# Kernel tuning notes

Measured on AMD Instinct MI355X. Metric: run time of the kernel, lower is better.

## Reference

```python
import jax, jax.numpy as jnp
import numpy as np

B, R, L, K, E, H, V, QV = 256, 6, 10, 49, 300, 512, 2001, 10000


def _lstm_dir(x, Wih, Whh, bih, bhh):
    # x: [N, L, E]; returns final hidden state [N, H] (PyTorch gate order i,f,g,o)
    N = x.shape[0]
    Hd = Whh.shape[1]
    b = bih + bhh

    def step(carry, xt):
        h, c = carry
        gates = xt @ Wih.T + h @ Whh.T + b
        i, f, g, o = jnp.split(gates, 4, axis=-1)
        c = jax.nn.sigmoid(f) * c + jax.nn.sigmoid(i) * jnp.tanh(g)
        h = jax.nn.sigmoid(o) * jnp.tanh(c)
        return (h, c), None

    init = (jnp.zeros((N, Hd), x.dtype), jnp.zeros((N, Hd), x.dtype))
    (h, _), _ = jax.lax.scan(step, init, jnp.swapaxes(x, 0, 1))
    return h


def setup_inputs() -> dict:
    key = jax.random.key(0)
    ks = jax.random.split(key, 40)
    s = 0.02
    d = {}
    d['img'] = jax.random.normal(ks[0], (B * R, K, H), jnp.float32)
    d['role_qs'] = jax.random.randint(ks[1], (B, R, L), 0, QV, jnp.int64)
    d['qword_emb'] = jax.random.normal(ks[2], (QV, E), jnp.float32) * s
    d['lstm_Wih_f'] = jax.random.normal(ks[3], (4 * H, E), jnp.float32) * s
    d['lstm_Whh_f'] = jax.random.normal(ks[4], (4 * H, H), jnp.float32) * s
    d['lstm_bih_f'] = jnp.zeros((4 * H,), jnp.float32)
    d['lstm_bhh_f'] = jnp.zeros((4 * H,), jnp.float32)
    d['lstm_Wih_b'] = jax.random.normal(ks[5], (4 * H, E), jnp.float32) * s
    d['lstm_Whh_b'] = jax.random.normal(ks[6], (4 * H, H), jnp.float32) * s
    d['lstm_bih_b'] = jnp.zeros((4 * H,), jnp.float32)
    d['lstm_bhh_b'] = jnp.zeros((4 * H,), jnp.float32)
    d['proj_W'] = jax.random.normal(ks[7], (H, 2 * H), jnp.float32) * s
    d['proj_b'] = jnp.zeros((H,), jnp.float32)
    d['vatt_vW'] = jax.random.normal(ks[8], (H, H), jnp.float32) * s
    d['vatt_vb'] = jnp.zeros((H,), jnp.float32)
    d['vatt_qW'] = jax.random.normal(ks[9], (H, H), jnp.float32) * s
    d['vatt_qb'] = jnp.zeros((H,), jnp.float32)
    d['vatt_oW'] = jax.random.normal(ks[10], (1, H), jnp.float32) * s
    d['vatt_ob'] = jnp.zeros((1,), jnp.float32)
    d['qnet_W'] = jax.random.normal(ks[11], (H, H), jnp.float32) * s
    d['qnet_b'] = jnp.zeros((H,), jnp.float32)
    d['vnet_W'] = jax.random.normal(ks[12], (H, H), jnp.float32) * s
    d['vnet_b'] = jnp.zeros((H,), jnp.float32)
    d['cls_W1'] = jax.random.normal(ks[13], (2 * H, H), jnp.float32) * s
    d['cls_b1'] = jnp.zeros((2 * H,), jnp.float32)
    d['cls_W2'] = jax.random.normal(ks[14], (V, 2 * H), jnp.float32) * s
    d['cls_b2'] = jnp.zeros((V,), jnp.float32)
    d['g0_W'] = jax.random.normal(ks[15], (H, 2 * H), jnp.float32) * s
    d['g0_b'] = jnp.zeros((H,), jnp.float32)
    d['g1_W'] = jax.random.normal(ks[16], (H, H), jnp.float32) * s
    d['g1_b'] = jnp.zeros((H,), jnp.float32)
    d['g2_W'] = jax.random.normal(ks[17], (H, H), jnp.float32) * s
    d['g2_b'] = jnp.zeros((H,), jnp.float32)
    d['g3_W'] = jax.random.normal(ks[18], (H, H), jnp.float32) * s
    d['g3_b'] = jnp.zeros((H,), jnp.float32)
    d['f0_W'] = jax.random.normal(ks[19], (H, H), jnp.float32) * s
    d['f0_b'] = jnp.zeros((H,), jnp.float32)
    d['f1_W'] = jax.random.normal(ks[20], (H, H), jnp.float32) * s
    d['f1_b'] = jnp.zeros((H,), jnp.float32)
    return d


def _forward(img, qword_emb,
             lstm_Wih_f, lstm_Whh_f, lstm_bih_f, lstm_bhh_f,
             lstm_Wih_b, lstm_Whh_b, lstm_bih_b, lstm_bhh_b,
             proj_W, proj_b, vatt_vW, vatt_vb, vatt_qW, vatt_qb, vatt_oW, vatt_ob,
             qnet_W, qnet_b, vnet_W, vnet_b, cls_W1, cls_b1, cls_W2, cls_b2,
             g0_W, g0_b, g1_W, g1_b, g2_W, g2_b, g3_W, g3_b,
             f0_W, f0_b, f1_W, f1_b, role_qs):
    relu = jax.nn.relu
    bsz, roles = role_qs.shape[0], role_qs.shape[1]
    toks = role_qs.reshape(-1, role_qs.shape[-1])          # [B*R, L]
    w_emb = qword_emb[toks]                                 # [B*R, L, E]
    # bidirectional LSTM final hidden states
    h_f = _lstm_dir(w_emb, lstm_Wih_f, lstm_Whh_f, lstm_bih_f, lstm_bhh_f)
    h_b = _lstm_dir(w_emb[:, ::-1, :], lstm_Wih_b, lstm_Whh_b, lstm_bih_b, lstm_bhh_b)
    q_emb = jnp.concatenate([h_f, h_b], axis=-1) @ proj_W.T + proj_b   # [B*R, H]
    # top-down attention over image regions
    v_proj = relu(img @ vatt_vW.T + vatt_vb)                # [B*R, K, H]
    q_proj = relu(q_emb @ vatt_qW.T + vatt_qb)              # [B*R, H]
    att_logits = (v_proj * q_proj[:, None, :]) @ vatt_oW.T + vatt_ob  # [B*R, K, 1]
    att = jax.nn.softmax(att_logits, axis=1)
    v_emb = jnp.sum(att * img, axis=1)                      # [B*R, H]
    # joint representation + answer classifier
    q_repr = relu(q_emb @ qnet_W.T + qnet_b)
    v_repr = relu(v_emb @ vnet_W.T + vnet_b)
    joint_repr = q_repr * v_repr                            # [B*R, H]
    logits = relu(joint_repr @ cls_W1.T + cls_b1) @ cls_W2.T + cls_b2  # [B*R, V]
    # relation network over pairwise role representations
    jr = joint_repr.reshape(bsz, roles, -1)                 # [B, R, H]
    r1 = jnp.broadcast_to(jr[:, None, :, :], (bsz, roles, roles, jr.shape[-1]))
    r2 = jnp.broadcast_to(jr[:, :, None, :], (bsz, roles, roles, jr.shape[-1]))
    cat = jnp.concatenate([r1, r2], axis=-1).reshape(-1, 2 * jr.shape[-1])  # [B*R*R, 2H]
    g = relu(cat @ g0_W.T + g0_b)
    g = relu(g @ g1_W.T + g1_b)
    g = relu(g @ g2_W.T + g2_b)
    g = relu(g @ g3_W.T + g3_b)
    g = g.reshape(bsz, roles * roles, -1).sum(axis=1)       # [B, H]
    rec = relu(g @ f0_W.T + f0_b) @ f1_W.T + f1_b           # [B, H]
    rec = rec / jnp.sqrt(jnp.sum(rec * rec, axis=1, keepdims=True))  # l2norm
    return logits, rec


def reference(img, role_qs, qword_emb,
              lstm_Wih_f, lstm_Whh_f, lstm_bih_f, lstm_bhh_f,
              lstm_Wih_b, lstm_Whh_b, lstm_bih_b, lstm_bhh_b,
              proj_W, proj_b, vatt_vW, vatt_vb, vatt_qW, vatt_qb, vatt_oW, vatt_ob,
              qnet_W, qnet_b, vnet_W, vnet_b, cls_W1, cls_b1, cls_W2, cls_b2,
              g0_W, g0_b, g1_W, g1_b, g2_W, g2_b, g3_W, g3_b,
              f0_W, f0_b, f1_W, f1_b):
    return _forward(img, qword_emb,
                    lstm_Wih_f, lstm_Whh_f, lstm_bih_f, lstm_bhh_f,
                    lstm_Wih_b, lstm_Whh_b, lstm_bih_b, lstm_bhh_b,
                    proj_W, proj_b, vatt_vW, vatt_vb, vatt_qW, vatt_qb, vatt_oW, vatt_ob,
                    qnet_W, qnet_b, vnet_W, vnet_b, cls_W1, cls_b1, cls_W2, cls_b2,
                    g0_W, g0_b, g1_W, g1_b, g2_W, g2_b, g3_W, g3_b,
                    f0_W, f0_b, f1_W, f1_b, role_qs)
```

## Files before the change

### kernel.cpp

```cpp
#include <hip/hip_runtime.h>
#include <hip/hip_bf16.h>
#include <math.h>

typedef __attribute__((ext_vector_type(8))) short short8;
typedef __attribute__((ext_vector_type(4))) float f32x4;

#define BT 64
#define KTILE 32
#define LSTR 40

__device__ __forceinline__ short8 cvt8(const float* x) {
    short8 r;
#pragma unroll
    for (int i = 0; i < 8; ++i) {
        __hip_bfloat16 b = __float2bfloat16(x[i]);
        r[i] = *reinterpret_cast<const short*>(&b);
    }
    return r;
}

__global__ __launch_bounds__(256)
void mfma_gemm_kernel(const float* __restrict__ A1, const int* __restrict__ idx1, int idx_stride,
                      int lda1, int k1,
                      const float* __restrict__ W1, int ldw1,
                      const float* __restrict__ A2, int lda2, int k2,
                      const float* __restrict__ W2, int ldw2,
                      const float* __restrict__ bias1, const float* __restrict__ bias2,
                      const float* __restrict__ mulvec, const float* __restrict__ mul,
                      float* __restrict__ C, int ldc, int M, int N, int do_relu, int mode)
{
    __shared__ short sA[2][BT][LSTR];
    __shared__ short sB[2][BT][LSTR];
    __shared__ float sred[BT][2];

    const int tid = threadIdx.x;
    int m0, n0, ch8 = 0;
    if (mode == 1) {
        const int xcd = blockIdx.x & 7;
        const int gi = xcd * 1176 + (blockIdx.x >> 3);
        m0 = (gi >> 3) << 6;
        ch8 = gi & 7;
        n0 = ch8 << 6;
    } else {
        m0 = blockIdx.y * BT;
        n0 = blockIdx.x * BT;
    }
    const int Ktot = k1 + k2;
    const int srow = tid >> 2;
    const int skq  = (tid & 3) << 3;
    const int lane = tid & 63;
    const int wave = tid >> 6;
    const int wr = (wave >> 1) << 5;
    const int wc = (wave & 1) << 5;
    const int l15 = lane & 15;
    const int lh  = lane >> 4;

    const int rg = min(m0 + srow, M - 1);
    const int arow = idx1 ? idx1[(size_t)rg * idx_stride] : rg;
    const int ng = min(n0 + srow, N - 1);

    f32x4 acc[2][2];
#pragma unroll
    for (int m = 0; m < 2; ++m)
#pragma unroll
        for (int n = 0; n < 2; ++n)
            acc[m][n] = (f32x4){0.f, 0.f, 0.f, 0.f};

    const int nt = (Ktot + KTILE - 1) / KTILE;
    float a[8], w[8];

    auto loadregs = [&](int t) {
        const int kb = t * KTILE;
        if (kb + KTILE <= k1) {
            const float* p = A1 + (size_t)arow * lda1 + kb + skq;
            float4 v0 = *(const float4*)p, v1 = *(const float4*)(p + 4);
            a[0]=v0.x; a[1]=v0.y; a[2]=v0.z; a[3]=v0.w; a[4]=v1.x; a[5]=v1.y; a[6]=v1.z; a[7]=v1.w;
            const float* q = W1 + (size_t)ng * ldw1 + kb + skq;
            float4 u0 = *(const float4*)q, u1 = *(const float4*)(q + 4);
            w[0]=u0.x; w[1]=u0.y; w[2]=u0.z; w[3]=u0.w; w[4]=u1.x; w[5]=u1.y; w[6]=u1.z; w[7]=u1.w;
        } else if (kb >= k1 && kb + KTILE <= Ktot) {
            const float* p = A2 + (size_t)rg * lda2 + (kb - k1) + skq;
            float4 v0 = *(const float4*)p, v1 = *(const float4*)(p + 4);
            a[0]=v0.x; a[1]=v0.y; a[2]=v0.z; a[3]=v0.w; a[4]=v1.x; a[5]=v1.y; a[6]=v1.z; a[7]=v1.w;
            const float* q = W2 + (size_t)ng * ldw2 + (kb - k1) + skq;
            float4 u0 = *(const float4*)q, u1 = *(const float4*)(q + 4);
            w[0]=u0.x; w[1]=u0.y; w[2]=u0.z; w[3]=u0.w; w[4]=u1.x; w[5]=u1.y; w[6]=u1.z; w[7]=u1.w;
        } else {
#pragma unroll
            for (int e = 0; e < 8; ++e) {
                int kg = kb + skq + e;
                float av = 0.f, wv = 0.f;
                if (kg < k1) {
                    av = A1[(size_t)arow * lda1 + kg];
                    wv = W1[(size_t)ng * ldw1 + kg];
                } else if (kg < Ktot) {
                    av = A2[(size_t)rg * lda2 + (kg - k1)];
                    wv = W2[(size_t)ng * ldw2 + (kg - k1)];
                }
                a[e] = av; w[e] = wv;
            }
        }
    };
    auto cvtwrite = [&](int buf) {
        *(short8*)&sA[buf][srow][skq] = cvt8(a);
        *(short8*)&sB[buf][srow][skq] = cvt8(w);
    };

    loadregs(0);
    cvtwrite(0);
    __syncthreads();

    for (int t = 0; t < nt; ++t) {
        const int cur = t & 1;
        if (t + 1 < nt) loadregs(t + 1);
        short8 af[2], bf[2];
#pragma unroll
        for (int m = 0; m < 2; ++m)
            af[m] = *(const short8*)&sA[cur][wr + (m << 4) + l15][lh << 3];
#pragma unroll
        for (int n = 0; n < 2; ++n)
            bf[n] = *(const short8*)&sB[cur][wc + (n << 4) + l15][lh << 3];
#pragma unroll
        for (int m = 0; m < 2; ++m)
#pragma unroll
            for (int n = 0; n < 2; ++n)
                acc[m][n] = __builtin_amdgcn_mfma_f32_16x16x32_bf16(af[m], bf[n], acc[m][n], 0, 0, 0);
        if (t + 1 < nt) cvtwrite(cur ^ 1);
        __syncthreads();
    }

    if (mode == 0) {
#pragma unroll
        for (int m = 0; m < 2; ++m) {
#pragma unroll
            for (int j = 0; j < 4; ++j) {
                const int r = m0 + wr + (m << 4) + (lh << 2) + j;
                if (r >= M) continue;
#pragma unroll
                for (int n = 0; n < 2; ++n) {
                    const int c = n0 + wc + (n << 4) + l15;
                    if (c >= N) continue;
                    float v = acc[m][n][j];
                    if (bias1) v += bias1[c];
                    if (bias2) v += bias2[c];
                    if (do_relu) v = fmaxf(v, 0.f);
                    if (mulvec) v *= mulvec[c];
                    if (mul) v *= mul[(size_t)r * ldc + c];
                    C[(size_t)r * ldc + c] = v;
                }
            }
        }
    } else {
#pragma unroll
        for (int m = 0; m < 2; ++m) {
#pragma unroll
            for (int j = 0; j < 4; ++j) {
                const int rloc = wr + (m << 4) + (lh << 2) + j;
                const int r = m0 + rloc;
                const size_t sqbase = (size_t)(r / 49) * ldc;
                float s = 0.f;
#pragma unroll
                for (int n = 0; n < 2; ++n) {
                    const int c = n0 + wc + (n << 4) + l15;
                    float v = acc[m][n][j] + bias1[c];
                    v = fmaxf(v, 0.f);
                    s += v * mul[sqbase + c];
                }
                s += __shfl_xor(s, 1, 64);
                s += __shfl_xor(s, 2, 64);
                s += __shfl_xor(s, 4, 64);
                s += __shfl_xor(s, 8, 64);
                if (l15 == 0) sred[rloc][wc >> 5] = s;
            }
        }
        __syncthreads();
        if (tid < BT)
            C[(size_t)(m0 + tid) * 8 + ch8] = sred[tid][0] + sred[tid][1];
    }
}

__global__ __launch_bounds__(256)
void lstm_reorder_kernel(const float* __restrict__ Wih, const float* __restrict__ Whh,
                         const float* __restrict__ bih, const float* __restrict__ bhh,
                         short* __restrict__ Wbf, float* __restrict__ bias_perm)
{
    int id = blockIdx.x * 256 + threadIdx.x;
    int c = id >> 9, k = id & 511;
    int src = (c & 3) * 512 + (c >> 2);
    {
        __hip_bfloat16 b = __float2bfloat16(Whh[(size_t)src * 512 + k]);
        Wbf[(size_t)c * 832 + k] = *(short*)&b;
    }
    if (k < 300) {
        __hip_bfloat16 b = __float2bfloat16(Wih[(size_t)src * 300 + k]);
        Wbf[(size_t)c * 832 + 512 + k] = *(short*)&b;
    } else if (k < 320) {
        Wbf[(size_t)c * 832 + 512 + k] = 0;
    }
    if (k == 0) bias_perm[c] = bih[src] + bhh[src];
}

__global__ __launch_bounds__(256)
void lstm_step2_kernel(const float* __restrict__ hF_in, const float* __restrict__ hB_in,
                       const short* __restrict__ WbfF, const short* __restrict__ WbfB,
                       const float* __restrict__ biasF, const float* __restrict__ biasB,
                       const float* __restrict__ emb, const int* __restrict__ toks,
                       int tF, int tB,
                       float* __restrict__ hF_out, float* __restrict__ hB_out,
                       float* __restrict__ cF, float* __restrict__ cB)
{
    __shared__ short sA[2][BT][LSTR];
    __shared__ short sB[2][BT][LSTR];
    const int dir = blockIdx.z;
    const float* h_in = dir ? hB_in : hF_in;
    const short* Wbf  = dir ? WbfB : WbfF;
    const float* bias_perm = dir ? biasB : biasF;
    float* h_out  = dir ? hB_out : hF_out;
    float* cstate = dir ? cB : cF;
    const int tt = dir ? tB : tF;

    const int tid = threadIdx.x;
    const int m0 = blockIdx.y << 6;
    const int n0 = blockIdx.x << 6;
    const int srow = tid >> 2, skq = (tid & 3) << 3;
    const int lane = tid & 63, wave = tid >> 6;
    const int wr = (wave >> 1) << 5, wc = (wave & 1) << 5;
    const int l15 = lane & 15, lh = lane >> 4;
    const int Ktot = 812;
    const int nt = 26;
    const int rg = m0 + srow;
    const int ng = n0 + srow;
    const int arow = toks[rg * 10 + tt];

    f32x4 acc[2][2];
#pragma unroll
    for (int m = 0; m < 2; ++m)
#pragma unroll
        for (int n = 0; n < 2; ++n)
            acc[m][n] = (f32x4){0.f, 0.f, 0.f, 0.f};

    float a[8];
    short8 wb;
    auto loadregs = [&](int t) {
        const int kb = t << 5;
        wb = *(const short8*)&Wbf[(size_t)ng * 832 + kb + skq];
        const int k0 = kb + skq;
        if (k0 + 8 <= 512) {
            const float* p = h_in + ((size_t)rg << 9) + k0;
            float4 v0 = *(const float4*)p, v1 = *(const float4*)(p + 4);
            a[0]=v0.x; a[1]=v0.y; a[2]=v0.z; a[3]=v0.w; a[4]=v1.x; a[5]=v1.y; a[6]=v1.z; a[7]=v1.w;
        } else if (k0 + 8 <= Ktot) {
            const float* p = emb + (size_t)arow * 300 + (k0 - 512);
            float4 v0 = *(const float4*)p, v1 = *(const float4*)(p + 4);
            a[0]=v0.x; a[1]=v0.y; a[2]=v0.z; a[3]=v0.w; a[4]=v1.x; a[5]=v1.y; a[6]=v1.z; a[7]=v1.w;
        } else {
#pragma unroll
            for (int e = 0; e < 8; ++e) {
                int kg = k0 + e;
                a[e] = (kg < 512) ? h_in[((size_t)rg << 9) + kg]
                                  : (kg < Ktot ? emb[(size_t)arow * 300 + (kg - 512)] : 0.f);
            }
        }
    };
    auto cvtwrite = [&](int buf) {
        *(short8*)&sA[buf][srow][skq] = cvt8(a);
        *(short8*)&sB[buf][srow][skq] = wb;
    };

    loadregs(0);
    cvtwrite(0);
    __syncthreads();
    for (int t = 0; t < nt; ++t) {
        const int cur = t & 1;
        if (t + 1 < nt) loadregs(t + 1);
        short8 af[2], bf[2];
#pragma unroll
        for (int m = 0; m < 2; ++m)
            af[m] = *(const short8*)&sA[cur][wr + (m << 4) + l15][lh << 3];
#pragma unroll
        for (int n = 0; n < 2; ++n)
            bf[n] = *(const short8*)&sB[cur][wc + (n << 4) + l15][lh << 3];
#pragma unroll
        for (int m = 0; m < 2; ++m)
#pragma unroll
            for (int n = 0; n < 2; ++n)
                acc[m][n] = __builtin_amdgcn_mfma_f32_16x16x32_bf16(af[m], bf[n], acc[m][n], 0, 0, 0);
        if (t + 1 < nt) cvtwrite(cur ^ 1);
        __syncthreads();
    }

#pragma unroll
    for (int n = 0; n < 2; ++n) {
        const int ccol = n0 + wc + (n << 4) + l15;
        const float bb = bias_perm[ccol];
        const int u = ccol >> 2;
#pragma unroll
        for (int m = 0; m < 2; ++m) {
#pragma unroll
            for (int j = 0; j < 4; ++j) {
                const int r = m0 + wr + (m << 4) + (lh << 2) + j;
                float v = acc[m][n][j] + bb;
                const int base = lane & ~3;
                float gi = __shfl(v, base, 64);
                float gf = __shfl(v, base | 1, 64);
                float gg = __shfl(v, base | 2, 64);
                float go = __shfl(v, base | 3, 64);
                if ((lane & 3) == 0) {
                    float si = 1.f / (1.f + expf(-gi));
                    float sf = 1.f / (1.f + expf(-gf));
                    float so = 1.f / (1.f + expf(-go));
                    size_t idx = ((size_t)r << 9) + u;
                    float cv = sf * cstate[idx] + si * tanhf(gg);
                    cstate[idx] = cv;
                    h_out[idx] = so * tanhf(cv);
                }
            }
        }
    }
}

__global__ __launch_bounds__(256)
void attn_vemb_kernel(const float* __restrict__ partial, const float* __restrict__ img,
                      float* __restrict__ v_emb)
{
    __shared__ float satt[49];
    const int n = blockIdx.x;
    const int tid = threadIdx.x;
    if (tid < 64) {
        float v = -1e30f;
        if (tid < 49) {
            const float* pp = partial + ((size_t)n * 49 + tid) * 8;
            v = ((pp[0] + pp[1]) + (pp[2] + pp[3])) + ((pp[4] + pp[5]) + (pp[6] + pp[7]));
        }
        float m = v;
#pragma unroll
        for (int off = 32; off; off >>= 1) m = fmaxf(m, __shfl_xor(m, off, 64));
        float e = (tid < 49) ? expf(v - m) : 0.f;
        float s = e;
#pragma unroll
        for (int off = 32; off; off >>= 1) s += __shfl_xor(s, off, 64);
        if (tid < 49) satt[tid] = e / s;
    }
    __syncthreads();
    const float2* ip = (const float2*)(img + (size_t)n * 49 * 512);
    float2 s2 = make_float2(0.f, 0.f);
    for (int k = 0; k < 49; ++k) {
        float2 v = ip[k * 256 + tid];
        float a = satt[k];
        s2.x = fmaf(a, v.x, s2.x);
        s2.y = fmaf(a, v.y, s2.y);
    }
    ((float2*)(v_emb + (size_t)n * 512))[tid] = s2;
}

__global__ __launch_bounds__(256)
void g0build_kernel(const float* __restrict__ P, const float* __restrict__ Q,
                    const float* __restrict__ b0, float* __restrict__ g0)
{
    int id = blockIdx.x * 256 + threadIdx.x;
    int cc = id & 511;
    int r = id >> 9;
    int j = r % 6;
    int t = r / 6;
    int i = t % 6;
    int b = t / 6;
    float v = P[((size_t)(b * 6 + j) << 9) + cc] + Q[((size_t)(b * 6 + i) << 9) + cc] + b0[cc];
    g0[id] = fmaxf(v, 0.f);
}

__global__ __launch_bounds__(256)
void gsum_kernel(const float* __restrict__ g, float* __restrict__ out)
{
    int id = blockIdx.x * 256 + threadIdx.x;
    int b = id >> 9, hh = id & 511;
    const float* p = g + (size_t)b * 36 * 512 + hh;
    float s = 0.f;
#pragma unroll
    for (int i = 0; i < 36; ++i) s += p[i * 512];
    out[id] = s;
}

__global__ __launch_bounds__(256)
void l2norm_kernel(const float* __restrict__ in, float* __restrict__ out)
{
    int b = blockIdx.x;
    int tid = threadIdx.x;
    float v0 = in[(size_t)b * 512 + tid];
    float v1 = in[(size_t)b * 512 + 256 + tid];
    float s = v0 * v0 + v1 * v1;
#pragma unroll
    for (int off = 32; off; off >>= 1) s += __shfl_down(s, off, 64);
    __shared__ float ps[4];
    if ((tid & 63) == 0) ps[tid >> 6] = s;
    __syncthreads();
    float tot = ps[0] + ps[1] + ps[2] + ps[3];
    float inv = 1.f / sqrtf(tot);
    out[(size_t)b * 512 + tid] = v0 * inv;
    out[(size_t)b * 512 + 256 + tid] = v1 * inv;
}

extern "C" void kernel_launch(void* const* d_in, const int* in_sizes, int n_in,
                              void* d_out, int out_size, void* d_ws, size_t ws_size,
                              hipStream_t stream)
{
    (void)in_sizes; (void)n_in; (void)out_size; (void)ws_size;
    const float* img    = (const float*)d_in[0];
    const int*   toks   = (const int*)d_in[1];
    const float* qword  = (const float*)d_in[2];
    const float* Wih_f  = (const float*)d_in[3];
    const float* Whh_f  = (const float*)d_in[4];
    const float* bih_f  = (const float*)d_in[5];
    const float* bhh_f  = (const float*)d_in[6];
    const float* Wih_b  = (const float*)d_in[7];
    const float* Whh_b  = (const float*)d_in[8];
    const float* bih_b  = (const float*)d_in[9];
    const float* bhh_b  = (const float*)d_in[10];
    const float* proj_W = (const float*)d_in[11];
    const float* proj_b = (const float*)d_in[12];
    const float* vatt_vW = (const float*)d_in[13];
    const float* vatt_vb = (const float*)d_in[14];
    const float* vatt_qW = (const float*)d_in[15];
    const float* vatt_qb = (const float*)d_in[16];
    const float* vatt_oW = (const float*)d_in[17];
    const float* qnet_W = (const float*)d_in[19];
    const float* qnet_b = (const float*)d_in[20];
    const float* vnet_W = (const float*)d_in[21];
    const float* vnet_b = (const float*)d_in[22];
    const float* cls_W1 = (const float*)d_in[23];
    const float* cls_b1 = (const float*)d_in[24];
    const float* cls_W2 = (const float*)d_in[25];
    const float* cls_b2 = (const float*)d_in[26];
    const float* g0_W   = (const float*)d_in[27];
    const float* g0_b   = (const float*)d_in[28];
    const float* g1_W   = (const float*)d_in[29];
    const float* g1_b   = (const float*)d_in[30];
    const float* g2_W   = (const float*)d_in[31];
    const float* g2_b   = (const float*)d_in[32];
    const float* g3_W   = (const float*)d_in[33];
    const float* g3_b   = (const float*)d_in[34];
    const float* f0_W   = (const float*)d_in[35];
    const float* f0_b   = (const float*)d_in[36];
    const float* f1_W   = (const float*)d_in[37];
    const float* f1_b   = (const float*)d_in[38];

    float* out_logits = (float*)d_out;
    float* out_rec    = (float*)d_out + 1536 * 2001;

    const size_t FB = 786432;
    float* zone = (float*)d_ws;
    float* gA    = zone;
    float* gB    = zone + 4718592;
    float* hid1  = zone + 9437184;
    float* Pb    = zone + 11010048;
    float* Qb    = zone + 11796480;
    float* gsumb = zone + 12582912;
    float* f0o   = zone + 12713984;
    float* rectb = zone + 12845056;
    float* p = zone + 12976128;
    auto alloc = [&](size_t nf) { float* q = p; p += nf; return q; };
    float* hP0   = alloc(FB);
    float* hP2   = alloc(FB);
    float* joint = alloc(FB);
    float* partial = alloc(602112);
    short* WbfF  = (short*)alloc(851968);
    short* WbfB  = (short*)alloc(851968);
    float* biasF = alloc(2048);
    float* biasB = alloc(2048);
    float* hP1 = gA;
    float* hP3 = gA + FB;
    float* cF  = gA + 2 * FB;
    float* cB  = gA + 3 * FB;
    float* q_emb  = Pb;
    float* swq    = hid1;
    float* q_repr = gA;
    float* v_emb  = gA + FB;

    auto gemm = [&](const float* A1, const int* idx1, int idxs, int lda1, int k1,
                    const float* W1, int ldw1,
                    const float* A2, int lda2, int k2, const float* W2, int ldw2,
                    const float* b1, const float* b2, const float* mv, const float* mulp,
                    float* Cp, int ldc, int M, int N, int relu) {
        dim3 g((N + BT - 1) / BT, (M + BT - 1) / BT);
        hipLaunchKernelGGL(mfma_gemm_kernel, g, dim3(256), 0, stream,
                           A1, idx1, idxs, lda1, k1, W1, ldw1, A2, lda2, k2, W2, ldw2,
                           b1, b2, mv, mulp, Cp, ldc, M, N, relu, 0);
    };

    const int NR = 1536;
    hipLaunchKernelGGL(lstm_reorder_kernel, dim3(4096), dim3(256), 0, stream,
                       Wih_f, Whh_f, bih_f, bhh_f, WbfF, biasF);
    hipLaunchKernelGGL(lstm_reorder_kernel, dim3(4096), dim3(256), 0, stream,
                       Wih_b, Whh_b, bih_b, bhh_b, WbfB, biasB);
    hipMemsetAsync(hP0, 0, FB * sizeof(float), stream);
    hipMemsetAsync(hP2, 0, FB * sizeof(float), stream);
    hipMemsetAsync(cF, 0, FB * sizeof(float), stream);
    hipMemsetAsync(cB, 0, FB * sizeof(float), stream);
    {
        float *fi = hP0, *fo = hP1, *bi = hP2, *bo = hP3;
        for (int t = 0; t < 10; ++t) {
            hipLaunchKernelGGL(lstm_step2_kernel, dim3(32, 24, 2), dim3(256), 0, stream,
                               fi, bi, WbfF, WbfB, biasF, biasB, qword, toks, t, 9 - t,
                               fo, bo, cF, cB);
            float* tmp = fi; fi = fo; fo = tmp;
            tmp = bi; bi = bo; bo = tmp;
        }
    }

    gemm(hP0, nullptr, 0, 512, 512, proj_W, 1024,
         hP2, 512, 512, proj_W + 512, 1024,
         proj_b, nullptr, nullptr, nullptr, q_emb, 512, NR, 512, 0);
    gemm(q_emb, nullptr, 0, 512, 512, vatt_qW, 512, nullptr, 0, 0, nullptr, 0,
         vatt_qb, nullptr, vatt_oW, nullptr, swq, 512, NR, 512, 1);
    hipLaunchKernelGGL(mfma_gemm_kernel, dim3(9408), dim3(256), 0, stream,
                       img, (const int*)nullptr, 0, 512, 512, vatt_vW, 512,
                       (const float*)nullptr, 0, 0, (const float*)nullptr, 0,
                       vatt_vb, (const float*)nullptr, (const float*)nullptr, swq,
                       partial, 512, 75264, 512, 0, 1);
    hipLaunchKernelGGL(attn_vemb_kernel, dim3(1536), dim3(256), 0, stream,
                       partial, img, v_emb);
    gemm(q_emb, nullptr, 0, 512, 512, qnet_W, 512, nullptr, 0, 0, nullptr, 0,
         qnet_b, nullptr, nullptr, nullptr, q_repr, 512, NR, 512, 1);
    gemm(v_emb, nullptr, 0, 512, 512, vnet_W, 512, nullptr, 0, 0, nullptr, 0,
         vnet_b, nullptr, nullptr, q_repr, joint, 512, NR, 512, 1);
    gemm(joint, nullptr, 0, 512, 512, cls_W1, 512, nullptr, 0, 0, nullptr, 0,
         cls_b1, nullptr, nullptr, nullptr, hid1, 1024, NR, 1024, 1);
    gemm(hid1, nullptr, 0, 1024, 1024, cls_W2, 1024, nullptr, 0, 0, nullptr, 0,
         cls_b2, nullptr, nullptr, nullptr, out_logits, 2001, NR, 2001, 0);
    gemm(joint, nullptr, 0, 512, 512, g0_W, 1024, nullptr, 0, 0, nullptr, 0,
         nullptr, nullptr, nullptr, nullptr, Pb, 512, NR, 512, 0);
    gemm(joint, nullptr, 0, 512, 512, g0_W + 512, 1024, nullptr, 0, 0, nullptr, 0,
         nullptr, nullptr, nullptr, nullptr, Qb, 512, NR, 512, 0);
    hipLaunchKernelGGL(g0build_kernel, dim3(18432), dim3(256), 0, stream, Pb, Qb, g0_b, gA);
    gemm(gA, nullptr, 0, 512, 512, g1_W, 512, nullptr, 0, 0, nullptr, 0,
         g1_b, nullptr, nullptr, nullptr, gB, 512, 9216, 512, 1);
    gemm(gB, nullptr, 0, 512, 512, g2_W, 512, nullptr, 0, 0, nullptr, 0,
         g2_b, nullptr, nullptr, nullptr, gA, 512, 9216, 512, 1);
    gemm(gA, nullptr, 0, 512, 512, g3_W, 512, nullptr, 0, 0, nullptr, 0,
         g3_b, nullptr, nullptr, nullptr, gB, 512, 9216, 512, 1);
    hipLaunchKernelGGL(gsum_kernel, dim3(512), dim3(256), 0, stream, gB, gsumb);
    gemm(gsumb, nullptr, 0, 512, 512, f0_W, 512, nullptr, 0, 0, nullptr, 0,
         f0_b, nullptr, nullptr, nullptr, f0o, 512, 256, 512, 1);
    gemm(f0o, nullptr, 0, 512, 512, f1_W, 512, nullptr, 0, 0, nullptr, 0,
         f1_b, nullptr, nullptr, nullptr, rectb, 512, 256, 512, 0);
    hipLaunchKernelGGL(l2norm_kernel, dim3(256), dim3(256), 0, stream, rectb, out_rec);
}
```

Measured before the change: 941.6 us.

## Store intermediate activations in bf16 and enlarge GEMM tiles to 128x64

Intermediate activations (LSTM hidden states, g-MLP buffers, joint and hidden layers) are now written and read as bf16 rather than fp32. The image tensor is pre-converted to bf16 when workspace permits. The GEMM and LSTM step kernels move from 64x64 to 128x64 tiles, with each wave computing 4x2 MFMA tiles. The goal is to halve activation memory traffic and conversion work and to raise per-block compute reuse, at the cost of an extra image conversion pass, more registers, and fewer blocks.

```diff
diff --git a/kernel.cpp b/kernel.cpp
--- a/kernel.cpp
+++ b/kernel.cpp
@@ -5,7 +5,6 @@
 typedef __attribute__((ext_vector_type(8))) short short8;
 typedef __attribute__((ext_vector_type(4))) float f32x4;
 
-#define BT 64
 #define KTILE 32
 #define LSTR 40
 
@@ -18,120 +17,152 @@
     }
     return r;
 }
-
-__global__ __launch_bounds__(256)
-void mfma_gemm_kernel(const float* __restrict__ A1, const int* __restrict__ idx1, int idx_stride,
-                      int lda1, int k1,
+__device__ __forceinline__ float bf2f(short s) {
+    unsigned int u = ((unsigned int)(unsigned short)s) << 16;
+    return __uint_as_float(u);
+}
+
+__global__ __launch_bounds__(256)
+void mfma_gemm_kernel(const float* __restrict__ A1f, int lda1, int k1,
                       const float* __restrict__ W1, int ldw1,
-                      const float* __restrict__ A2, int lda2, int k2,
+                      const float* __restrict__ A2f, int lda2, int k2,
                       const float* __restrict__ W2, int ldw2,
                       const float* __restrict__ bias1, const float* __restrict__ bias2,
                       const float* __restrict__ mulvec, const float* __restrict__ mul,
-                      float* __restrict__ C, int ldc, int M, int N, int do_relu, int mode)
-{
-    __shared__ short sA[2][BT][LSTR];
-    __shared__ short sB[2][BT][LSTR];
-    __shared__ float sred[BT][2];
+                      float* __restrict__ C, int ldc, int M, int N,
+                      int do_relu, int mode, int abits, int c_bf16)
+{
+    __shared__ short sA[2][128][LSTR];
+    __shared__ short sB[2][64][LSTR];
+    __shared__ float sred[128][2];
 
     const int tid = threadIdx.x;
     int m0, n0, ch8 = 0;
     if (mode == 1) {
         const int xcd = blockIdx.x & 7;
-        const int gi = xcd * 1176 + (blockIdx.x >> 3);
-        m0 = (gi >> 3) << 6;
+        const int gi = xcd * 588 + (blockIdx.x >> 3);
+        m0 = (gi >> 3) << 7;
         ch8 = gi & 7;
         n0 = ch8 << 6;
     } else {
-        m0 = blockIdx.y * BT;
-        n0 = blockIdx.x * BT;
-    }
+        m0 = blockIdx.y << 7;
+        n0 = blockIdx.x << 6;
+    }
+    const short* A1b = (const short*)A1f;
+    const short* A2b = (const short*)A2f;
     const int Ktot = k1 + k2;
-    const int srow = tid >> 2;
-    const int skq  = (tid & 3) << 3;
-    const int lane = tid & 63;
-    const int wave = tid >> 6;
-    const int wr = (wave >> 1) << 5;
+    const int nt = (Ktot + KTILE - 1) / KTILE;
+    const int lane = tid & 63, wave = tid >> 6;
+    const int wr = (wave >> 1) << 6;
     const int wc = (wave & 1) << 5;
-    const int l15 = lane & 15;
-    const int lh  = lane >> 4;
-
-    const int rg = min(m0 + srow, M - 1);
-    const int arow = idx1 ? idx1[(size_t)rg * idx_stride] : rg;
-    const int ng = min(n0 + srow, N - 1);
-
-    f32x4 acc[2][2];
-#pragma unroll
-    for (int m = 0; m < 2; ++m)
-#pragma unroll
-        for (int n = 0; n < 2; ++n)
-            acc[m][n] = (f32x4){0.f, 0.f, 0.f, 0.f};
-
-    const int nt = (Ktot + KTILE - 1) / KTILE;
-    float a[8], w[8];
-
-    auto loadregs = [&](int t) {
-        const int kb = t * KTILE;
-        if (kb + KTILE <= k1) {
-            const float* p = A1 + (size_t)arow * lda1 + kb + skq;
-            float4 v0 = *(const float4*)p, v1 = *(const float4*)(p + 4);
-            a[0]=v0.x; a[1]=v0.y; a[2]=v0.z; a[3]=v0.w; a[4]=v1.x; a[5]=v1.y; a[6]=v1.z; a[7]=v1.w;
-            const float* q = W1 + (size_t)ng * ldw1 + kb + skq;
+    const int l15 = lane & 15, lh = lane >> 4;
+    const int rowA = tid >> 1, kA = (tid & 1) << 4;
+    const int rgA = min(m0 + rowA, M - 1);
+    const int rowW = tid >> 2, kW = (tid & 3) << 3;
+    const int ngW = min(n0 + rowW, N - 1);
+
+    f32x4 acc[4][2];
+#pragma unroll
+    for (int m = 0; m < 4; ++m)
+#pragma unroll
+        for (int n = 0; n < 2; ++n) acc[m][n] = (f32x4){0.f, 0.f, 0.f, 0.f};
+
+    short8 aS0, aS1, wS;
+    auto loadA = [&](int t) {
+        const int k0 = t * KTILE + kA;
+        if (k0 + 16 <= k1) {
+            if (abits & 1) {
+                const short* p = A1b + (size_t)rgA * lda1 + k0;
+                aS0 = *(const short8*)p; aS1 = *(const short8*)(p + 8);
+            } else {
+                const float* p = A1f + (size_t)rgA * lda1 + k0;
+                float4 v0 = *(const float4*)p, v1 = *(const float4*)(p + 4);
+                float4 v2 = *(const float4*)(p + 8), v3 = *(const float4*)(p + 12);
+                float t0[8] = {v0.x, v0.y, v0.z, v0.w, v1.x, v1.y, v1.z, v1.w};
+                float t1[8] = {v2.x, v2.y, v2.z, v2.w, v3.x, v3.y, v3.z, v3.w};
+                aS0 = cvt8(t0); aS1 = cvt8(t1);
+            }
+        } else if (k0 >= k1 && k0 + 16 <= Ktot) {
+            const int kk = k0 - k1;
+            if (abits & 2) {
+                const short* p = A2b + (size_t)rgA * lda2 + kk;
+                aS0 = *(const short8*)p; aS1 = *(const short8*)(p + 8);
+            } else {
+                const float* p = A2f + (size_t)rgA * lda2 + kk;
+                float4 v0 = *(const float4*)p, v1 = *(const float4*)(p + 4);
+                float4 v2 = *(const float4*)(p + 8), v3 = *(const float4*)(p + 12);
+                float t0[8] = {v0.x, v0.y, v0.z, v0.w, v1.x, v1.y, v1.z, v1.w};
+                float t1[8] = {v2.x, v2.y, v2.z, v2.w, v3.x, v3.y, v3.z, v3.w};
+                aS0 = cvt8(t0); aS1 = cvt8(t1);
+            }
+        } else {
+            float tmp[16];
+#pragma unroll
+            for (int e = 0; e < 16; ++e) {
+                const int kg = k0 + e;
+                float v = 0.f;
+                if (kg < k1) v = (abits & 1) ? bf2f(A1b[(size_t)rgA * lda1 + kg]) : A1f[(size_t)rgA * lda1 + kg];
+                else if (kg < Ktot) v = (abits & 2) ? bf2f(A2b[(size_t)rgA * lda2 + (kg - k1)]) : A2f[(size_t)rgA * lda2 + (kg - k1)];
+                tmp[e] = v;
+            }
+            aS0 = cvt8(tmp); aS1 = cvt8(tmp + 8);
+        }
+    };
+    auto loadW = [&](int t) {
+        const int k0 = t * KTILE + kW;
+        if (k0 + 8 <= k1) {
+            const float* q = W1 + (size_t)ngW * ldw1 + k0;
             float4 u0 = *(const float4*)q, u1 = *(const float4*)(q + 4);
-            w[0]=u0.x; w[1]=u0.y; w[2]=u0.z; w[3]=u0.w; w[4]=u1.x; w[5]=u1.y; w[6]=u1.z; w[7]=u1.w;
-        } else if (kb >= k1 && kb + KTILE <= Ktot) {
-            const float* p = A2 + (size_t)rg * lda2 + (kb - k1) + skq;
-            float4 v0 = *(const float4*)p, v1 = *(const float4*)(p + 4);
-            a[0]=v0.x; a[1]=v0.y; a[2]=v0.z; a[3]=v0.w; a[4]=v1.x; a[5]=v1.y; a[6]=v1.z; a[7]=v1.w;
-            const float* q = W2 + (size_t)ng * ldw2 + (kb - k1) + skq;
+            float t0[8] = {u0.x, u0.y, u0.z, u0.w, u1.x, u1.y, u1.z, u1.w};
+            wS = cvt8(t0);
+        } else if (k0 >= k1 && k0 + 8 <= Ktot) {
+            const float* q = W2 + (size_t)ngW * ldw2 + (k0 - k1);
             float4 u0 = *(const float4*)q, u1 = *(const float4*)(q + 4);
-            w[0]=u0.x; w[1]=u0.y; w[2]=u0.z; w[3]=u0.w; w[4]=u1.x; w[5]=u1.y; w[6]=u1.z; w[7]=u1.w;
+            float t0[8] = {u0.x, u0.y, u0.z, u0.w, u1.x, u1.y, u1.z, u1.w};
+            wS = cvt8(t0);
         } else {
+            float tmp[8];
 #pragma unroll
             for (int e = 0; e < 8; ++e) {
-                int kg = kb + skq + e;
-                float av = 0.f, wv = 0.f;
-                if (kg < k1) {
-                    av = A1[(size_t)arow * lda1 + kg];
-                    wv = W1[(size_t)ng * ldw1 + kg];
-                } else if (kg < Ktot) {
-                    av = A2[(size_t)rg * lda2 + (kg - k1)];
-                    wv = W2[(size_t)ng * ldw2 + (kg - k1)];
-                }
-                a[e] = av; w[e] = wv;
-            }
+                const int kg = k0 + e;
+                float v = 0.f;
+                if (kg < k1) v = W1[(size_t)ngW * ldw1 + kg];
+                else if (kg < Ktot) v = W2[(size_t)ngW * ldw2 + (kg - k1)];
+                tmp[e] = v;
+            }
+            wS = cvt8(tmp);
         }
     };
-    auto cvtwrite = [&](int buf) {
-        *(short8*)&sA[buf][srow][skq] = cvt8(a);
-        *(short8*)&sB[buf][srow][skq] = cvt8(w);
+    auto writeS = [&](int buf) {
+        *(short8*)&sA[buf][rowA][kA] = aS0;
+        *(short8*)&sA[buf][rowA][kA + 8] = aS1;
+        *(short8*)&sB[buf][rowW][kW] = wS;
     };
 
-    loadregs(0);
-    cvtwrite(0);
+    loadA(0); loadW(0); writeS(0);
     __syncthreads();
-
     for (int t = 0; t < nt; ++t) {
         const int cur = t & 1;
-        if (t + 1 < nt) loadregs(t + 1);
-        short8 af[2], bf[2];
-#pragma unroll
-        for (int m = 0; m < 2; ++m)
+        if (t + 1 < nt) { loadA(t + 1); loadW(t + 1); }
+        short8 af[4], bfv[2];
+#pragma unroll
+        for (int m = 0; m < 4; ++m)
             af[m] = *(const short8*)&sA[cur][wr + (m << 4) + l15][lh << 3];
 #pragma unroll
         for (int n = 0; n < 2; ++n)
-            bf[n] = *(const short8*)&sB[cur][wc + (n << 4) + l15][lh << 3];
-#pragma unroll
-        for (int m = 0; m < 2; ++m)
+            bfv[n] = *(const short8*)&sB[cur][wc + (n << 4) + l15][lh << 3];
+#pragma unroll
+        for (int m = 0; m < 4; ++m)
 #pragma unroll
             for (int n = 0; n < 2; ++n)
-                acc[m][n] = __builtin_amdgcn_mfma_f32_16x16x32_bf16(af[m], bf[n], acc[m][n], 0, 0, 0);
-        if (t + 1 < nt) cvtwrite(cur ^ 1);
+                acc[m][n] = __builtin_amdgcn_mfma_f32_16x16x32_bf16(af[m], bfv[n], acc[m][n], 0, 0, 0);
+        if (t + 1 < nt) writeS(cur ^ 1);
         __syncthreads();
     }
 
     if (mode == 0) {
 #pragma unroll
-        for (int m = 0; m < 2; ++m) {
+        for (int m = 0; m < 4; ++m) {
 #pragma unroll
             for (int j = 0; j < 4; ++j) {
                 const int r = m0 + wr + (m << 4) + (lh << 2) + j;
@@ -146,13 +177,18 @@
                     if (do_relu) v = fmaxf(v, 0.f);
                     if (mulvec) v *= mulvec[c];
                     if (mul) v *= mul[(size_t)r * ldc + c];
-                    C[(size_t)r * ldc + c] = v;
+                    if (c_bf16) {
+                        __hip_bfloat16 b = __float2bfloat16(v);
+                        ((short*)C)[(size_t)r * ldc + c] = *(short*)&b;
+                    } else {
+                        C[(size_t)r * ldc + c] = v;
+                    }
                 }
             }
         }
     } else {
 #pragma unroll
-        for (int m = 0; m < 2; ++m) {
+        for (int m = 0; m < 4; ++m) {
 #pragma unroll
             for (int j = 0; j < 4; ++j) {
                 const int rloc = wr + (m << 4) + (lh << 2) + j;
@@ -174,7 +210,7 @@
             }
         }
         __syncthreads();
-        if (tid < BT)
+        if (tid < 128)
             C[(size_t)(m0 + tid) * 8 + ch8] = sred[tid][0] + sred[tid][1];
     }
 }
@@ -201,91 +237,94 @@
 }
 
 __global__ __launch_bounds__(256)
-void lstm_step2_kernel(const float* __restrict__ hF_in, const float* __restrict__ hB_in,
+void lstm_step2_kernel(const short* __restrict__ hF_in, const short* __restrict__ hB_in,
                        const short* __restrict__ WbfF, const short* __restrict__ WbfB,
                        const float* __restrict__ biasF, const float* __restrict__ biasB,
                        const float* __restrict__ emb, const int* __restrict__ toks,
                        int tF, int tB,
-                       float* __restrict__ hF_out, float* __restrict__ hB_out,
+                       short* __restrict__ hF_out, short* __restrict__ hB_out,
                        float* __restrict__ cF, float* __restrict__ cB)
 {
-    __shared__ short sA[2][BT][LSTR];
-    __shared__ short sB[2][BT][LSTR];
+    __shared__ short sA[2][128][LSTR];
+    __shared__ short sB[2][64][LSTR];
     const int dir = blockIdx.z;
-    const float* h_in = dir ? hB_in : hF_in;
+    const short* h_in = dir ? hB_in : hF_in;
     const short* Wbf  = dir ? WbfB : WbfF;
     const float* bias_perm = dir ? biasB : biasF;
-    float* h_out  = dir ? hB_out : hF_out;
+    short* h_out  = dir ? hB_out : hF_out;
     float* cstate = dir ? cB : cF;
     const int tt = dir ? tB : tF;
 
     const int tid = threadIdx.x;
-    const int m0 = blockIdx.y << 6;
+    const int m0 = blockIdx.y << 7;
     const int n0 = blockIdx.x << 6;
-    const int srow = tid >> 2, skq = (tid & 3) << 3;
     const int lane = tid & 63, wave = tid >> 6;
-    const int wr = (wave >> 1) << 5, wc = (wave & 1) << 5;
+    const int wr = (wave >> 1) << 6, wc = (wave & 1) << 5;
     const int l15 = lane & 15, lh = lane >> 4;
-    const int Ktot = 812;
+    const int rowA = tid >> 1, kA = (tid & 1) << 4;
+    const int rgA = m0 + rowA;
+    const int rowW = tid >> 2, kW = (tid & 3) << 3;
+    const int ngW = n0 + rowW;
     const int nt = 26;
-    const int rg = m0 + srow;
-    const int ng = n0 + srow;
-    const int arow = toks[rg * 10 + tt];
-
-    f32x4 acc[2][2];
-#pragma unroll
-    for (int m = 0; m < 2; ++m)
-#pragma unroll
-        for (int n = 0; n < 2; ++n)
-            acc[m][n] = (f32x4){0.f, 0.f, 0.f, 0.f};
-
-    float a[8];
-    short8 wb;
-    auto loadregs = [&](int t) {
-        const int kb = t << 5;
-        wb = *(const short8*)&Wbf[(size_t)ng * 832 + kb + skq];
-        const int k0 = kb + skq;
-        if (k0 + 8 <= 512) {
-            const float* p = h_in + ((size_t)rg << 9) + k0;
-            float4 v0 = *(const float4*)p, v1 = *(const float4*)(p + 4);
-            a[0]=v0.x; a[1]=v0.y; a[2]=v0.z; a[3]=v0.w; a[4]=v1.x; a[5]=v1.y; a[6]=v1.z; a[7]=v1.w;
-        } else if (k0 + 8 <= Ktot) {
+    const int arow = toks[rgA * 10 + tt];
+
+    f32x4 acc[4][2];
+#pragma unroll
+    for (int m = 0; m < 4; ++m)
+#pragma unroll
+        for (int n = 0; n < 2; ++n) acc[m][n] = (f32x4){0.f, 0.f, 0.f, 0.f};
+
+    short8 aS0, aS1, wS;
+    auto loadA = [&](int t) {
+        const int k0 = (t << 5) + kA;
+        if (k0 + 16 <= 512) {
+            const short* p = h_in + (size_t)rgA * 512 + k0;
+            aS0 = *(const short8*)p; aS1 = *(const short8*)(p + 8);
+        } else if (k0 >= 512 && k0 + 16 <= 812) {
             const float* p = emb + (size_t)arow * 300 + (k0 - 512);
             float4 v0 = *(const float4*)p, v1 = *(const float4*)(p + 4);
-            a[0]=v0.x; a[1]=v0.y; a[2]=v0.z; a[3]=v0.w; a[4]=v1.x; a[5]=v1.y; a[6]=v1.z; a[7]=v1.w;
+            float4 v2 = *(const float4*)(p + 8), v3 = *(const float4*)(p + 12);
+            float t0[8] = {v0.x, v0.y, v0.z, v0.w, v1.x, v1.y, v1.z, v1.w};
+            float t1[8] = {v2.x, v2.y, v2.z, v2.w, v3.x, v3.y, v3.z, v3.w};
+            aS0 = cvt8(t0); aS1 = cvt8(t1);
         } else {
-#pragma unroll
-            for (int e = 0; e < 8; ++e) {
-                int kg = k0 + e;
-                a[e] = (kg < 512) ? h_in[((size_t)rg << 9) + kg]
-                                  : (kg < Ktot ? emb[(size_t)arow * 300 + (kg - 512)] : 0.f);
-            }
+            float tmp[16];
+#pragma unroll
+            for (int e = 0; e < 16; ++e) {
+                const int kg = k0 + e;
+                tmp[e] = (kg < 812) ? ((kg < 512) ? bf2f(h_in[(size_t)rgA * 512 + kg])
+                                                  : emb[(size_t)arow * 300 + (kg - 512)]) : 0.f;
+            }
+            aS0 = cvt8(tmp); aS1 = cvt8(tmp + 8);
         }
     };
-    auto cvtwrite = [&](int buf) {
-        *(short8*)&sA[buf][srow][skq] = cvt8(a);
-        *(short8*)&sB[buf][srow][skq] = wb;
+    auto loadW = [&](int t) {
+        wS = *(const short8*)&Wbf[(size_t)ngW * 832 + (t << 5) + kW];
     };
-
-    loadregs(0);
-    cvtwrite(0);
+    auto writeS = [&](int buf) {
+        *(short8*)&sA[buf][rowA][kA] = aS0;
+        *(short8*)&sA[buf][rowA][kA + 8] = aS1;
+        *(short8*)&sB[buf][rowW][kW] = wS;
+    };
+
+    loadA(0); loadW(0); writeS(0);
     __syncthreads();
     for (int t = 0; t < nt; ++t) {
         const int cur = t & 1;
-        if (t + 1 < nt) loadregs(t + 1);
-        short8 af[2], bf[2];
-#pragma unroll
-        for (int m = 0; m < 2; ++m)
+        if (t + 1 < nt) { loadA(t + 1); loadW(t + 1); }
+        short8 af[4], bfv[2];
+#pragma unroll
+        for (int m = 0; m < 4; ++m)
             af[m] = *(const short8*)&sA[cur][wr + (m << 4) + l15][lh << 3];
 #pragma unroll
         for (int n = 0; n < 2; ++n)
-            bf[n] = *(const short8*)&sB[cur][wc + (n << 4) + l15][lh << 3];
-#pragma unroll
-        for (int m = 0; m < 2; ++m)
+            bfv[n] = *(const short8*)&sB[cur][wc + (n << 4) + l15][lh << 3];
+#pragma unroll
+        for (int m = 0; m < 4; ++m)
 #pragma unroll
             for (int n = 0; n < 2; ++n)
-                acc[m][n] = __builtin_amdgcn_mfma_f32_16x16x32_bf16(af[m], bf[n], acc[m][n], 0, 0, 0);
-        if (t + 1 < nt) cvtwrite(cur ^ 1);
+                acc[m][n] = __builtin_amdgcn_mfma_f32_16x16x32_bf16(af[m], bfv[n], acc[m][n], 0, 0, 0);
+        if (t + 1 < nt) writeS(cur ^ 1);
         __syncthreads();
     }
 
@@ -295,7 +334,7 @@
         const float bb = bias_perm[ccol];
         const int u = ccol >> 2;
 #pragma unroll
-        for (int m = 0; m < 2; ++m) {
+        for (int m = 0; m < 4; ++m) {
 #pragma unroll
             for (int j = 0; j < 4; ++j) {
                 const int r = m0 + wr + (m << 4) + (lh << 2) + j;
@@ -312,7 +351,9 @@
                     size_t idx = ((size_t)r << 9) + u;
                     float cv = sf * cstate[idx] + si * tanhf(gg);
                     cstate[idx] = cv;
-                    h_out[idx] = so * tanhf(cv);
+                    float hv = so * tanhf(cv);
+                    __hip_bfloat16 b = __float2bfloat16(hv);
+                    h_out[idx] = *(short*)&b;
                 }
             }
         }
@@ -320,8 +361,17 @@
 }
 
 __global__ __launch_bounds__(256)
+void imgcvt_kernel(const float* __restrict__ img, short* __restrict__ out)
+{
+    size_t i = ((size_t)blockIdx.x * 256 + threadIdx.x) * 8;
+    float4 a = *(const float4*)(img + i), b = *(const float4*)(img + i + 4);
+    float t[8] = {a.x, a.y, a.z, a.w, b.x, b.y, b.z, b.w};
+    *(short8*)(out + i) = cvt8(t);
+}
+
+__global__ __launch_bounds__(256)
 void attn_vemb_kernel(const float* __restrict__ partial, const float* __restrict__ img,
-                      float* __restrict__ v_emb)
+                      const short* __restrict__ imgb, float* __restrict__ v_emb)
 {
     __shared__ float satt[49];
     const int n = blockIdx.x;
@@ -342,20 +392,30 @@
         if (tid < 49) satt[tid] = e / s;
     }
     __syncthreads();
-    const float2* ip = (const float2*)(img + (size_t)n * 49 * 512);
     float2 s2 = make_float2(0.f, 0.f);
-    for (int k = 0; k < 49; ++k) {
-        float2 v = ip[k * 256 + tid];
-        float a = satt[k];
-        s2.x = fmaf(a, v.x, s2.x);
-        s2.y = fmaf(a, v.y, s2.y);
+    if (imgb) {
+        const unsigned int* ip = (const unsigned int*)(imgb + (size_t)n * 49 * 512);
+        for (int k = 0; k < 49; ++k) {
+            unsigned int v = ip[k * 256 + tid];
+            float a = satt[k];
+            s2.x = fmaf(a, bf2f((short)(v & 0xffff)), s2.x);
+            s2.y = fmaf(a, bf2f((short)(v >> 16)), s2.y);
+        }
+    } else {
+        const float2* ip = (const float2*)(img + (size_t)n * 49 * 512);
+        for (int k = 0; k < 49; ++k) {
+            float2 v = ip[k * 256 + tid];
+            float a = satt[k];
+            s2.x = fmaf(a, v.x, s2.x);
+            s2.y = fmaf(a, v.y, s2.y);
+        }
     }
     ((float2*)(v_emb + (size_t)n * 512))[tid] = s2;
 }
 
 __global__ __launch_bounds__(256)
 void g0build_kernel(const float* __restrict__ P, const float* __restrict__ Q,
-                    const float* __restrict__ b0, float* __restrict__ g0)
+                    const float* __restrict__ b0, short* __restrict__ g0)
 {
     int id = blockIdx.x * 256 + threadIdx.x;
     int cc = id & 511;
@@ -365,18 +425,20 @@
     int i = t % 6;
     int b = t / 6;
     float v = P[((size_t)(b * 6 + j) << 9) + cc] + Q[((size_t)(b * 6 + i) << 9) + cc] + b0[cc];
-    g0[id] = fmaxf(v, 0.f);
-}
-
-__global__ __launch_bounds__(256)
-void gsum_kernel(const float* __restrict__ g, float* __restrict__ out)
+    v = fmaxf(v, 0.f);
+    __hip_bfloat16 h = __float2bfloat16(v);
+    g0[id] = *(short*)&h;
+}
+
+__global__ __launch_bounds__(256)
+void gsum_kernel(const short* __restrict__ g, float* __restrict__ out)
 {
     int id = blockIdx.x * 256 + threadIdx.x;
     int b = id >> 9, hh = id & 511;
-    const float* p = g + (size_t)b * 36 * 512 + hh;
+    const short* p = g + (size_t)b * 36 * 512 + hh;
     float s = 0.f;
 #pragma unroll
-    for (int i = 0; i < 36; ++i) s += p[i * 512];
+    for (int i = 0; i < 36; ++i) s += bf2f(p[i * 512]);
     out[id] = s;
 }
 
@@ -403,7 +465,7 @@
                               void* d_out, int out_size, void* d_ws, size_t ws_size,
                               hipStream_t stream)
 {
-    (void)in_sizes; (void)n_in; (void)out_size; (void)ws_size;
+    (void)in_sizes; (void)n_in; (void)out_size;
     const float* img    = (const float*)d_in[0];
     const int*   toks   = (const int*)d_in[1];
     const float* qword  = (const float*)d_in[2];
@@ -466,8 +528,12 @@
     short* WbfB  = (short*)alloc(851968);
     float* biasF = alloc(2048);
     float* biasB = alloc(2048);
-    float* hP1 = gA;
-    float* hP3 = gA + FB;
+    const size_t TOPF = 17645568;
+    const size_t IMGBF = 19267584;
+    const bool useimgbf = ws_size >= (TOPF + IMGBF) * sizeof(float);
+    short* imgbf = (short*)(zone + TOPF);
+    short* hP1 = (short*)gA;
+    short* hP3 = (short*)(gA + FB);
     float* cF  = gA + 2 * FB;
     float* cB  = gA + 3 * FB;
     float* q_emb  = Pb;
@@ -475,15 +541,14 @@
     float* q_repr = gA;
     float* v_emb  = gA + FB;
 
-    auto gemm = [&](const float* A1, const int* idx1, int idxs, int lda1, int k1,
-                    const float* W1, int ldw1,
+    auto gemm = [&](const float* A1, int lda1, int k1, const float* W1, int ldw1,
                     const float* A2, int lda2, int k2, const float* W2, int ldw2,
                     const float* b1, const float* b2, const float* mv, const float* mulp,
-                    float* Cp, int ldc, int M, int N, int relu) {
-        dim3 g((N + BT - 1) / BT, (M + BT - 1) / BT);
+                    float* Cp, int ldc, int M, int N, int relu, int abits, int cbf) {
+        dim3 g((N + 63) / 64, (M + 127) / 128);
         hipLaunchKernelGGL(mfma_gemm_kernel, g, dim3(256), 0, stream,
-                           A1, idx1, idxs, lda1, k1, W1, ldw1, A2, lda2, k2, W2, ldw2,
-                           b1, b2, mv, mulp, Cp, ldc, M, N, relu, 0);
+                           A1, lda1, k1, W1, ldw1, A2, lda2, k2, W2, ldw2,
+                           b1, b2, mv, mulp, Cp, ldc, M, N, relu, 0, abits, cbf);
     };
 
     const int NR = 1536;
@@ -491,56 +556,58 @@
                        Wih_f, Whh_f, bih_f, bhh_f, WbfF, biasF);
     hipLaunchKernelGGL(lstm_reorder_kernel, dim3(4096), dim3(256), 0, stream,
                        Wih_b, Whh_b, bih_b, bhh_b, WbfB, biasB);
-    hipMemsetAsync(hP0, 0, FB * sizeof(float), stream);
-    hipMemsetAsync(hP2, 0, FB * sizeof(float), stream);
+    if (useimgbf)
+        hipLaunchKernelGGL(imgcvt_kernel, dim3(18816), dim3(256), 0, stream, img, imgbf);
+    hipMemsetAsync(hP0, 0, FB * sizeof(short), stream);
+    hipMemsetAsync(hP2, 0, FB * sizeof(short), stream);
     hipMemsetAsync(cF, 0, FB * sizeof(float), stream);
     hipMemsetAsync(cB, 0, FB * sizeof(float), stream);
     {
-        float *fi = hP0, *fo = hP1, *bi = hP2, *bo = hP3;
+        short *fi = (short*)hP0, *fo = hP1, *bi = (short*)hP2, *bo = hP3;
         for (int t = 0; t < 10; ++t) {
-            hipLaunchKernelGGL(lstm_step2_kernel, dim3(32, 24, 2), dim3(256), 0, stream,
+            hipLaunchKernelGGL(lstm_step2_kernel, dim3(32, 12, 2), dim3(256), 0, stream,
                                fi, bi, WbfF, WbfB, biasF, biasB, qword, toks, t, 9 - t,
                                fo, bo, cF, cB);
-            float* tmp = fi; fi = fo; fo = tmp;
+            short* tmp = fi; fi = fo; fo = tmp;
             tmp = bi; bi = bo; bo = tmp;
         }
     }
 
-    gemm(hP0, nullptr, 0, 512, 512, proj_W, 1024,
-         hP2, 512, 512, proj_W + 512, 1024,
-         proj_b, nullptr, nullptr, nullptr, q_emb, 512, NR, 512, 0);
-    gemm(q_emb, nullptr, 0, 512, 512, vatt_qW, 512, nullptr, 0, 0, nullptr, 0,
-         vatt_qb, nullptr, vatt_oW, nullptr, swq, 512, NR, 512, 1);
-    hipLaunchKernelGGL(mfma_gemm_kernel, dim3(9408), dim3(256), 0, stream,
-                       img, (const int*)nullptr, 0, 512, 512, vatt_vW, 512,
+    gemm(hP0, 512, 512, proj_W, 1024, hP2, 512, 512, proj_W + 512, 1024,
+         proj_b, nullptr, nullptr, nullptr, q_emb, 512, NR, 512, 0, 3, 1);
+    gemm(q_emb, 512, 512, vatt_qW, 512, nullptr, 0, 0, nullptr, 0,
+         vatt_qb, nullptr, vatt_oW, nullptr, swq, 512, NR, 512, 1, 1, 0);
+    hipLaunchKernelGGL(mfma_gemm_kernel, dim3(4704), dim3(256), 0, stream,
+                       useimgbf ? (const float*)imgbf : img, 512, 512, vatt_vW, 512,
                        (const float*)nullptr, 0, 0, (const float*)nullptr, 0,
                        vatt_vb, (const float*)nullptr, (const float*)nullptr, swq,
-                       partial, 512, 75264, 512, 0, 1);
+                       partial, 512, 75264, 512, 0, 1, useimgbf ? 1 : 0, 0);
     hipLaunchKernelGGL(attn_vemb_kernel, dim3(1536), dim3(256), 0, stream,
-                       partial, img, v_emb);
-    gemm(q_emb, nullptr, 0, 512, 512, qnet_W, 512, nullptr, 0, 0, nullptr, 0,
-         qnet_b, nullptr, nullptr, nullptr, q_repr, 512, NR, 512, 1);
-    gemm(v_emb, nullptr, 0, 512, 512, vnet_W, 512, nullptr, 0, 0, nullptr, 0,
-         vnet_b, nullptr, nullptr, q_repr, joint, 512, NR, 512, 1);
-    gemm(joint, nullptr, 0, 512, 512, cls_W1, 512, nullptr, 0, 0, nullptr, 0,
-         cls_b1, nullptr, nullptr, nullptr, hid1, 1024, NR, 1024, 1);
-    gemm(hid1, nullptr, 0, 1024, 1024, cls_W2, 1024, nullptr, 0, 0, nullptr, 0,
-         cls_b2, nullptr, nullptr, nullptr, out_logits, 2001, NR, 2001, 0);
-    gemm(joint, nullptr, 0, 512, 512, g0_W, 1024, nullptr, 0, 0, nullptr, 0,
-         nullptr, nullptr, nullptr, nullptr, Pb, 512, NR, 512, 0);
-    gemm(joint, nullptr, 0, 512, 512, g0_W + 512, 1024, nullptr, 0, 0, nullptr, 0,
-         nullptr, nullptr, nullptr, nullptr, Qb, 512, NR, 512, 0);
-    hipLaunchKernelGGL(g0build_kernel, dim3(18432), dim3(256), 0, stream, Pb, Qb, g0_b, gA);
-    gemm(gA, nullptr, 0, 512, 512, g1_W, 512, nullptr, 0, 0, nullptr, 0,
-         g1_b, nullptr, nullptr, nullptr, gB, 512, 9216, 512, 1);
-    gemm(gB, nullptr, 0, 512, 512, g2_W, 512, nullptr, 0, 0, nullptr, 0,
-         g2_b, nullptr, nullptr, nullptr, gA, 512, 9216, 512, 1);
-    gemm(gA, nullptr, 0, 512, 512, g3_W, 512, nullptr, 0, 0, nullptr, 0,
-         g3_b, nullptr, nullptr, nullptr, gB, 512, 9216, 512, 1);
-    hipLaunchKernelGGL(gsum_kernel, dim3(512), dim3(256), 0, stream, gB, gsumb);
-    gemm(gsumb, nullptr, 0, 512, 512, f0_W, 512, nullptr, 0, 0, nullptr, 0,
-         f0_b, nullptr, nullptr, nullptr, f0o, 512, 256, 512, 1);
-    gemm(f0o, nullptr, 0, 512, 512, f1_W, 512, nullptr, 0, 0, nullptr, 0,
-         f1_b, nullptr, nullptr, nullptr, rectb, 512, 256, 512, 0);
+                       partial, img, useimgbf ? imgbf : (const short*)nullptr, v_emb);
+    gemm(q_emb, 512, 512, qnet_W, 512, nullptr, 0, 0, nullptr, 0,
+         qnet_b, nullptr, nullptr, nullptr, q_repr, 512, NR, 512, 1, 1, 0);
+    gemm(v_emb, 512, 512, vnet_W, 512, nullptr, 0, 0, nullptr, 0,
+         vnet_b, nullptr, nullptr, q_repr, joint, 512, NR, 512, 1, 0, 1);
+    gemm(joint, 512, 512, cls_W1, 512, nullptr, 0, 0, nullptr, 0,
+         cls_b1, nullptr, nullptr, nullptr, hid1, 1024, NR, 1024, 1, 1, 1);
+    gemm(hid1, 1024, 1024, cls_W2, 1024, nullptr, 0, 0, nullptr, 0,
+         cls_b2, nullptr, nullptr, nullptr, out_logits, 2001, NR, 2001, 0, 1, 0);
+    gemm(joint, 512, 512, g0_W, 1024, nullptr, 0, 0, nullptr, 0,
+         nullptr, nullptr, nullptr, nullptr, Pb, 512, NR, 512, 0, 1, 0);
+    gemm(joint, 512, 512, g0_W + 512, 1024, nullptr, 0, 0, nullptr, 0,
+         nullptr, nullptr, nullptr, nullptr, Qb, 512, NR, 512, 0, 1, 0);
+    hipLaunchKernelGGL(g0build_kernel, dim3(18432), dim3(256), 0, stream,
+                       Pb, Qb, g0_b, (short*)gA);
+    gemm(gA, 512, 512, g1_W, 512, nullptr, 0, 0, nullptr, 0,
+         g1_b, nullptr, nullptr, nullptr, gB, 512, 9216, 512, 1, 1, 1);
+    gemm(gB, 512, 512, g2_W, 512, nullptr, 0, 0, nullptr, 0,
+         g2_b, nullptr, nullptr, nullptr, gA, 512, 9216, 512, 1, 1, 1);
+    gemm(gA, 512, 512, g3_W, 512, nullptr, 0, 0, nullptr, 0,
+         g3_b, nullptr, nullptr, nullptr, gB, 512, 9216, 512, 1, 1, 1);
+    hipLaunchKernelGGL(gsum_kernel, dim3(512), dim3(256), 0, stream, (const short*)gB, gsumb);
+    gemm(gsumb, 512, 512, f0_W, 512, nullptr, 0, 0, nullptr, 0,
+         f0_b, nullptr, nullptr, nullptr, f0o, 512, 256, 512, 1, 0, 0);
+    gemm(f0o, 512, 512, f1_W, 512, nullptr, 0, 0, nullptr, 0,
+         f1_b, nullptr, nullptr, nullptr, rectb, 512, 256, 512, 0, 0, 0);
     hipLaunchKernelGGL(l2norm_kernel, dim3(256), dim3(256), 0, stream, rectb, out_rec);
 }
```

New measurement: 1.049 ms. +11.4%, slower.
